# Kernel optimization log

Measured on AMD Instinct MI355X. Metric: run time of the kernel, lower is better.

Reference implementation:

```python
import jax, jax.numpy as jnp
import numpy as np

N, D = 16384, 64


def setup_inputs() -> dict:
    key = jax.random.key(0)
    k1, k2, k3, k4, k5 = jax.random.split(key, 5)
    x = jax.random.normal(k1, (N, D), dtype=jnp.float32)
    # labels in {-1, +1}
    y = jnp.sign(jax.random.normal(k2, (N,), dtype=jnp.float32))
    y = jnp.where(y == 0, 1.0, y)
    alpha = jax.random.uniform(k3, (N, 1), dtype=jnp.float32)
    xi = jax.random.uniform(k4, (N, 1), dtype=jnp.float32)
    b = jax.random.uniform(k5, (1,), dtype=jnp.float32, minval=-1.0, maxval=1.0)
    return {"x": x, "y": y, "alpha": alpha, "xi": xi, "b": b,
            "coeff": 1, "degree": 3, "C": 1, "lambd": 1}


def reference(x, y, alpha, xi, b, coeff, degree, C, lambd):
    a = jax.nn.relu(alpha)          # (N,1)
    xr = jax.nn.relu(xi)            # (N,1)
    # polynomial kernel Gram matrix: (x @ x.T + coeff)^degree  -> (N,N)
    K = (x @ x.T + coeff) ** degree
    # sum_j alpha_j * y_j * K_ij  (weighted row reduction)
    s = K @ (a * y[:, None])        # (N,1)
    left = y[:, None] * (s + b)     # (N,1)
    right = 1.0 - xr                # (N,1)
    loss = (0.5 * jnp.sum(jnp.abs(a))
            + C * jnp.sum(xr)
            + lambd * jnp.mean(left - right))
    return loss
```

## Files before the change

kernel.cpp:

```cpp
#include <hip/hip_runtime.h>

#define N_SAMP 16384
#define D_FEAT 64
#define TILE 128
#define NTILE 128
#define SPLIT 8
#define NPAIR (NTILE / 2)
#define NBLOCKS (NPAIR * SPLIT)
#define TPP (NTILE + 1)
#define SEG_BASE (TPP / SPLIT)
#define SEG_REM (TPP % SPLIT)

typedef __attribute__((ext_vector_type(8))) short bf16x8;
typedef __attribute__((ext_vector_type(4))) float f32x4;
typedef __attribute__((ext_vector_type(2))) float f32x2;
typedef __attribute__((ext_vector_type(4))) unsigned short u16x4;

__device__ __forceinline__ unsigned short f2bf_rne(float f) {
  union { float f; unsigned u; } v;
  v.f = f;
  unsigned u = v.u;
  return (unsigned short)((u + 0x7FFFu + ((u >> 16) & 1u)) >> 16);
}

__global__ __launch_bounds__(256) void prep_kernel(
    const float* __restrict__ x, const float* __restrict__ y,
    const float* __restrict__ alpha, const float* __restrict__ xi,
    unsigned short* __restrict__ xb, float4* __restrict__ psums) {
  int t = blockIdx.x * 256 + threadIdx.x;
  int base = t * 4;
  int row = base >> 6;
  float yv = y[row];
  float4 v = *(const float4*)(x + base);
  u16x4 o;
  o.x = f2bf_rne(v.x * yv);
  o.y = f2bf_rne(v.y * yv);
  o.z = f2bf_rne(v.z * yv);
  o.w = f2bf_rne(v.w * yv);
  *(u16x4*)(xb + base) = o;

  if (blockIdx.x < (N_SAMP / 256)) {
    float a = fmaxf(alpha[t], 0.0f);
    float xr = fmaxf(xi[t], 0.0f);
    float yy = y[t];
#pragma unroll
    for (int off = 32; off > 0; off >>= 1) {
      a += __shfl_down(a, off, 64);
      xr += __shfl_down(xr, off, 64);
      yy += __shfl_down(yy, off, 64);
    }
    __shared__ float ra[4], rx[4], ry[4];
    int wv = threadIdx.x >> 6;
    if ((threadIdx.x & 63) == 0) {
      ra[wv] = a;
      rx[wv] = xr;
      ry[wv] = yy;
    }
    __syncthreads();
    if (threadIdx.x == 0)
      psums[blockIdx.x] =
          make_float4(ra[0] + ra[1] + ra[2] + ra[3],
                      rx[0] + rx[1] + rx[2] + rx[3],
                      ry[0] + ry[1] + ry[2] + ry[3], 0.0f);
  }
}

__global__ __launch_bounds__(256, 2) void tile_kernel(
    const unsigned short* __restrict__ xb,
    const float* __restrict__ alpha,
    const float* __restrict__ y,
    const int* __restrict__ coeffp,
    const int* __restrict__ degp,
    float* __restrict__ partials) {
  __shared__ float wred[4];

  const int tid = threadIdx.x;
  const int lane = tid & 63;
  const int wv = tid >> 6;
  const int wm = wv >> 1;
  const int wn = wv & 1;
  const int lr = lane & 15;
  const int q = lane >> 4;

  const int p = blockIdx.x >> 3;
  const int sb = blockIdx.x & (SPLIT - 1);
  const int i1 = p, i2 = NTILE - 1 - p;
  const int cnt1 = NTILE - p;
  const int g0 = sb * SEG_BASE + (sb < SEG_REM ? sb : SEG_REM);
  const int gcnt = SEG_BASE + (sb < SEG_REM ? 1 : 0);

  auto g_to_ij = [&](int g, int& i, int& j) {
    if (g < cnt1) {
      i = i1;
      j = p + g;
    } else {
      i = i2;
      j = i2 + (g - cnt1);
    }
  };

  const char* xbytes = (const char*)xb;
  const float fco = (float)coeffp[0];
  const int deg = degp[0];

  f32x2 yr[4][2], ar[4][2];
  auto load_rows = [&](int ic) {
#pragma unroll
    for (int mt = 0; mt < 4; ++mt) {
      int idx = ic * TILE + wm * 64 + mt * 16 + q * 4;
      float4 yv = *(const float4*)(y + idx);
      float4 av = *(const float4*)(alpha + idx);
      yr[mt][0] = (f32x2){yv.x, yv.y};
      yr[mt][1] = (f32x2){yv.z, yv.w};
      ar[mt][0] = (f32x2){fmaxf(av.x, 0.0f), fmaxf(av.y, 0.0f)};
      ar[mt][1] = (f32x2){fmaxf(av.z, 0.0f), fmaxf(av.w, 0.0f)};
    }
  };

  bf16x8 af[4][2];
  auto read_af_g = [&](int rowtile) {
    const char* base = xbytes + (((size_t)(rowtile * TILE + wm * 64)) << 7);
#pragma unroll
    for (int mt = 0; mt < 4; ++mt) {
      int r = mt * 16 + lr;
#pragma unroll
      for (int kc = 0; kc < 2; ++kc)
        af[mt][kc] = *(const bf16x8*)(base + (r << 7) + ((kc * 4 + q) << 4));
    }
  };

  f32x2 rsum[4][2];
#pragma unroll
  for (int mt = 0; mt < 4; ++mt)
    for (int h = 0; h < 2; ++h) rsum[mt][h] = (f32x2){0.0f, 0.0f};
  float lane_total = 0.0f;

  auto flush_rsum = [&]() {
#pragma unroll
    for (int mt = 0; mt < 4; ++mt) {
      f32x2 s = rsum[mt][0] * ar[mt][0] + rsum[mt][1] * ar[mt][1];
      lane_total += s.x + s.y;
      rsum[mt][0] = (f32x2){0.0f, 0.0f};
      rsum[mt][1] = (f32x2){0.0f, 0.0f};
    }
  };

  f32x4 acc[4][4];
  float ycolP[4], wcolP[4];
  bool diagP = false;
  bool have_prev = false;

  auto epilogue_prev = [&]() {
    if (deg == 3) {
      if (diagP) {
#pragma unroll
        for (int nt = 0; nt < 4; ++nt) {
          f32x2 cs = {0.0f, 0.0f};
#pragma unroll
          for (int mt = 0; mt < 4; ++mt) {
#pragma unroll
            for (int h = 0; h < 2; ++h) {
              f32x2 T = {acc[mt][nt][2 * h], acc[mt][nt][2 * h + 1]};
              f32x2 T2 = T * T;
              cs += T2 * T;
            }
          }
          lane_total = fmaf(cs.x + cs.y, wcolP[nt], lane_total);
        }
      } else {
#pragma unroll
        for (int nt = 0; nt < 4; ++nt) {
          f32x2 cs = {0.0f, 0.0f};
#pragma unroll
          for (int mt = 0; mt < 4; ++mt) {
#pragma unroll
            for (int h = 0; h < 2; ++h) {
              f32x2 T = {acc[mt][nt][2 * h], acc[mt][nt][2 * h + 1]};
              f32x2 T2 = T * T;
              f32x2 P = T2 * T;
              cs += P;
              rsum[mt][h] += P;
            }
          }
          lane_total = fmaf(cs.x + cs.y, wcolP[nt], lane_total);
        }
      }
    } else {
#pragma unroll
      for (int nt = 0; nt < 4; ++nt) {
        float cs = 0.0f;
#pragma unroll
        for (int mt = 0; mt < 4; ++mt) {
          float ys[4] = {yr[mt][0].x, yr[mt][0].y, yr[mt][1].x, yr[mt][1].y};
          float as[4] = {ar[mt][0].x, ar[mt][0].y, ar[mt][1].x, ar[mt][1].y};
#pragma unroll
          for (int rg = 0; rg < 4; ++rg) {
            float T = acc[mt][nt][rg];
            float pw = 1.0f;
            for (int d = 0; d < deg; ++d) pw *= T;
            if (!(deg & 1)) pw *= ys[rg] * ycolP[nt];
            cs += pw;
            if (!diagP) lane_total += pw * as[rg];
          }
        }
        lane_total = fmaf(cs, wcolP[nt], lane_total);
      }
    }
  };

  {
    int i0, j0;
    g_to_ij(g0, i0, j0);
    load_rows(i0);
    read_af_g(i0);
  }
  int icur;
  {
    int j0;
    g_to_ij(g0, icur, j0);
  }

  for (int it = 0; it < gcnt; ++it) {
    int g = g0 + it;
    int i, j;
    g_to_ij(g, i, j);

    const char* bbase = xbytes + (((size_t)(j * TILE + wn * 64)) << 7);
    bf16x8 bfr[4][2];
#pragma unroll
    for (int nt = 0; nt < 4; ++nt) {
      int rr = nt * 16 + lr;
#pragma unroll
      for (int kc = 0; kc < 2; ++kc)
        bfr[nt][kc] = *(const bf16x8*)(bbase + (rr << 7) + ((kc * 4 + q) << 4));
    }

    float ycolN[4], wrawN[4];
#pragma unroll
    for (int nt = 0; nt < 4; ++nt) {
      int jj = j * TILE + wn * 64 + nt * 16 + lr;
      ycolN[nt] = y[jj];
      wrawN[nt] = alpha[jj];
    }

    if (have_prev) epilogue_prev();

    if (i != icur) {
      flush_rsum();
      load_rows(i);
      read_af_g(i);
      icur = i;
    }

    float ysc[4];
#pragma unroll
    for (int nt = 0; nt < 4; ++nt) ysc[nt] = ycolN[nt] * fco;

#pragma unroll
    for (int mt = 0; mt < 4; ++mt) {
#pragma unroll
      for (int nt = 0; nt < 4; ++nt) {
        f32x2 lo = yr[mt][0] * ysc[nt];
        f32x2 hi = yr[mt][1] * ysc[nt];
        acc[mt][nt][0] = lo.x;
        acc[mt][nt][1] = lo.y;
        acc[mt][nt][2] = hi.x;
        acc[mt][nt][3] = hi.y;
      }
    }

#pragma unroll
    for (int kc = 0; kc < 2; ++kc) {
#pragma unroll
      for (int mt = 0; mt < 4; ++mt) {
#pragma unroll
        for (int nt = 0; nt < 4; ++nt) {
          acc[mt][nt] = __builtin_amdgcn_mfma_f32_16x16x32_bf16(
              af[mt][kc], bfr[nt][kc], acc[mt][nt], 0, 0, 0);
        }
      }
    }

#pragma unroll
    for (int nt = 0; nt < 4; ++nt) {
      ycolP[nt] = ycolN[nt];
      wcolP[nt] = fmaxf(wrawN[nt], 0.0f);
    }
    diagP = (j == i);
    have_prev = true;
  }

  epilogue_prev();
  flush_rsum();

#pragma unroll
  for (int off = 32; off > 0; off >>= 1)
    lane_total += __shfl_down(lane_total, off, 64);
  if (lane == 0) wred[wv] = lane_total;
  __syncthreads();
  if (tid == 0)
    partials[blockIdx.x] = wred[0] + wred[1] + wred[2] + wred[3];
}

__global__ __launch_bounds__(256) void finalize_kernel(
    const float* __restrict__ partials,
    const float4* __restrict__ psums,
    const float* __restrict__ bp,
    const int* __restrict__ Cp,
    const int* __restrict__ lamp,
    float* __restrict__ out) {
  double tsum = 0.0, sa = 0.0, sx = 0.0, sy = 0.0;
  for (int i = threadIdx.x; i < NBLOCKS; i += 256) tsum += (double)partials[i];
  if (threadIdx.x < (N_SAMP / 256)) {
    float4 v = psums[threadIdx.x];
    sa = (double)v.x;
    sx = (double)v.y;
    sy = (double)v.z;
  }
#pragma unroll
  for (int off = 32; off > 0; off >>= 1) {
    tsum += __shfl_down(tsum, off, 64);
    sa += __shfl_down(sa, off, 64);
    sx += __shfl_down(sx, off, 64);
    sy += __shfl_down(sy, off, 64);
  }
  __shared__ double red[4][4];
  int wv = threadIdx.x >> 6;
  if ((threadIdx.x & 63) == 0) {
    red[wv][0] = tsum;
    red[wv][1] = sa;
    red[wv][2] = sx;
    red[wv][3] = sy;
  }
  __syncthreads();
  if (threadIdx.x == 0) {
    double T = red[0][0] + red[1][0] + red[2][0] + red[3][0];
    double A = red[0][1] + red[1][1] + red[2][1] + red[3][1];
    double X = red[0][2] + red[1][2] + red[2][2] + red[3][2];
    double Y = red[0][3] + red[1][3] + red[2][3] + red[3][3];
    double b = (double)bp[0];
    double Cc = (double)Cp[0];
    double lam = (double)lamp[0];
    double mean = (T + b * Y - (double)N_SAMP + X) / (double)N_SAMP;
    out[0] = (float)(0.5 * A + Cc * X + lam * mean);
  }
}

extern "C" void kernel_launch(void* const* d_in, const int* in_sizes, int n_in,
                              void* d_out, int out_size, void* d_ws,
                              size_t ws_size, hipStream_t stream) {
  const float* x = (const float*)d_in[0];
  const float* y = (const float*)d_in[1];
  const float* alpha = (const float*)d_in[2];
  const float* xi = (const float*)d_in[3];
  const float* b = (const float*)d_in[4];
  const int* coeff = (const int*)d_in[5];
  const int* degree = (const int*)d_in[6];
  const int* C = (const int*)d_in[7];
  const int* lambd = (const int*)d_in[8];

  unsigned short* xb = (unsigned short*)d_ws;
  char* pbase = (char*)d_ws + (size_t)N_SAMP * D_FEAT * 2;
  float* partials = (float*)pbase;
  float4* psums = (float4*)(pbase + ((NBLOCKS * 4 + 255) & ~255));

  prep_kernel<<<(N_SAMP * D_FEAT) / (4 * 256), 256, 0, stream>>>(x, y, alpha,
                                                                 xi, xb, psums);

  tile_kernel<<<NBLOCKS, 256, 0, stream>>>(xb, alpha, y, coeff, degree,
                                           partials);

  finalize_kernel<<<1, 256, 0, stream>>>(partials, psums, b, C, lambd,
                                         (float*)d_out);
}
```

Measured before the change: 111.0 us.

## Double-buffer B-tile and column loads one iteration ahead of MFMA

Restructures the main tile loop into a two-way unrolled ping-pong that issues global loads of the next tile's B fragments, y and alpha before running the current epilogue and MFMAs. This is meant to hide global load latency behind the epilogue and matrix work. It also raises wave priority around the MFMA block with s_setprio. The cost is a second set of fragment registers, which may raise VGPR pressure and lower occupancy.

```diff
diff --git a/kernel.cpp b/kernel.cpp
--- a/kernel.cpp
+++ b/kernel.cpp
@@ -208,86 +208,103 @@
     }
   };
 
-  {
-    int i0, j0;
-    g_to_ij(g0, i0, j0);
-    load_rows(i0);
-    read_af_g(i0);
-  }
-  int icur;
-  {
-    int j0;
-    g_to_ij(g0, icur, j0);
-  }
-
-  for (int it = 0; it < gcnt; ++it) {
-    int g = g0 + it;
-    int i, j;
-    g_to_ij(g, i, j);
-
-    const char* bbase = xbytes + (((size_t)(j * TILE + wn * 64)) << 7);
-    bf16x8 bfr[4][2];
-#pragma unroll
-    for (int nt = 0; nt < 4; ++nt) {
-      int rr = nt * 16 + lr;
-#pragma unroll
-      for (int kc = 0; kc < 2; ++kc)
-        bfr[nt][kc] = *(const bf16x8*)(bbase + (rr << 7) + ((kc * 4 + q) << 4));
-    }
-
-    float ycolN[4], wrawN[4];
-#pragma unroll
-    for (int nt = 0; nt < 4; ++nt) {
-      int jj = j * TILE + wn * 64 + nt * 16 + lr;
-      ycolN[nt] = y[jj];
-      wrawN[nt] = alpha[jj];
-    }
-
-    if (have_prev) epilogue_prev();
-
-    if (i != icur) {
-      flush_rsum();
-      load_rows(i);
-      read_af_g(i);
-      icur = i;
-    }
-
-    float ysc[4];
-#pragma unroll
-    for (int nt = 0; nt < 4; ++nt) ysc[nt] = ycolN[nt] * fco;
-
-#pragma unroll
-    for (int mt = 0; mt < 4; ++mt) {
-#pragma unroll
-      for (int nt = 0; nt < 4; ++nt) {
-        f32x2 lo = yr[mt][0] * ysc[nt];
-        f32x2 hi = yr[mt][1] * ysc[nt];
-        acc[mt][nt][0] = lo.x;
-        acc[mt][nt][1] = lo.y;
-        acc[mt][nt][2] = hi.x;
-        acc[mt][nt][3] = hi.y;
-      }
-    }
-
-#pragma unroll
-    for (int kc = 0; kc < 2; ++kc) {
-#pragma unroll
-      for (int mt = 0; mt < 4; ++mt) {
-#pragma unroll
-        for (int nt = 0; nt < 4; ++nt) {
-          acc[mt][nt] = __builtin_amdgcn_mfma_f32_16x16x32_bf16(
-              af[mt][kc], bfr[nt][kc], acc[mt][nt], 0, 0, 0);
-        }
-      }
-    }
-
-#pragma unroll
-    for (int nt = 0; nt < 4; ++nt) {
-      ycolP[nt] = ycolN[nt];
-      wcolP[nt] = fmaxf(wrawN[nt], 0.0f);
-    }
-    diagP = (j == i);
-    have_prev = true;
+#define ISSUE_LOADS(JN, YC, WR, BF)                                      \
+  {                                                                      \
+    _Pragma("unroll") for (int nt = 0; nt < 4; ++nt) {                   \
+      int jj = (JN)*TILE + wn * 64 + nt * 16 + lr;                       \
+      YC[nt] = y[jj];                                                    \
+      WR[nt] = alpha[jj];                                                \
+    }                                                                    \
+    const char* bb = xbytes + (((size_t)((JN)*TILE + wn * 64)) << 7);    \
+    _Pragma("unroll") for (int nt = 0; nt < 4; ++nt) {                   \
+      int rr = nt * 16 + lr;                                             \
+      _Pragma("unroll") for (int kc = 0; kc < 2; ++kc)                   \
+          BF[nt][kc] =                                                   \
+              *(const bf16x8*)(bb + (rr << 7) + ((kc * 4 + q) << 4));    \
+    }                                                                    \
+  }
+
+#define INIT_MFMA(YC, BF)                                                \
+  {                                                                      \
+    float ysc[4];                                                        \
+    _Pragma("unroll") for (int nt = 0; nt < 4; ++nt) ysc[nt] =           \
+        YC[nt] * fco;                                                    \
+    _Pragma("unroll") for (int mt = 0; mt < 4; ++mt)                     \
+        _Pragma("unroll") for (int nt = 0; nt < 4; ++nt) {               \
+      f32x2 lo = yr[mt][0] * ysc[nt];                                    \
+      f32x2 hi = yr[mt][1] * ysc[nt];                                    \
+      acc[mt][nt][0] = lo.x;                                             \
+      acc[mt][nt][1] = lo.y;                                             \
+      acc[mt][nt][2] = hi.x;                                             \
+      acc[mt][nt][3] = hi.y;                                             \
+    }                                                                    \
+    __builtin_amdgcn_s_setprio(1);                                       \
+    _Pragma("unroll") for (int kc = 0; kc < 2; ++kc)                     \
+        _Pragma("unroll") for (int mt = 0; mt < 4; ++mt)                 \
+            _Pragma("unroll") for (int nt = 0; nt < 4; ++nt)             \
+                acc[mt][nt] = __builtin_amdgcn_mfma_f32_16x16x32_bf16(   \
+                    af[mt][kc], BF[nt][kc], acc[mt][nt], 0, 0, 0);       \
+    __builtin_amdgcn_s_setprio(0);                                       \
+  }
+
+#define ROTATE(YC, WR, DIAG)                                             \
+  {                                                                      \
+    _Pragma("unroll") for (int nt = 0; nt < 4; ++nt) {                   \
+      ycolP[nt] = YC[nt];                                                \
+      wcolP[nt] = fmaxf(WR[nt], 0.0f);                                   \
+    }                                                                    \
+    diagP = (DIAG);                                                      \
+  }
+
+  float ycA[4], wrA[4], ycB[4], wrB[4];
+  bf16x8 bfA[4][2], bfB[4][2];
+
+  int icur, jfirst;
+  g_to_ij(g0, icur, jfirst);
+  ISSUE_LOADS(jfirst, ycA, wrA, bfA);
+  load_rows(icur);
+  read_af_g(icur);
+
+  for (int it = 0; it < gcnt; it += 2) {
+    {
+      int g = g0 + it;
+      int i, j;
+      g_to_ij(g, i, j);
+      if (it + 1 < gcnt) {
+        int in_, jn;
+        g_to_ij(g + 1, in_, jn);
+        ISSUE_LOADS(jn, ycB, wrB, bfB);
+      }
+      if (have_prev) epilogue_prev();
+      if (i != icur) {
+        flush_rsum();
+        load_rows(i);
+        read_af_g(i);
+        icur = i;
+      }
+      INIT_MFMA(ycA, bfA);
+      ROTATE(ycA, wrA, j == i);
+      have_prev = true;
+    }
+    if (it + 1 < gcnt) {
+      int g = g0 + it + 1;
+      int i, j;
+      g_to_ij(g, i, j);
+      if (it + 2 < gcnt) {
+        int in_, jn;
+        g_to_ij(g + 1, in_, jn);
+        ISSUE_LOADS(jn, ycA, wrA, bfA);
+      }
+      epilogue_prev();
+      if (i != icur) {
+        flush_rsum();
+        load_rows(i);
+        read_af_g(i);
+        icur = i;
+      }
+      INIT_MFMA(ycB, bfB);
+      ROTATE(ycB, wrB, j == i);
+    }
   }
 
   epilogue_prev();
```

Measured after the change: 153.1 us. 1.38x slower.
